# Kernel tuning notes

Hardware: AMD Instinct MI355X
Metric: run time of the kernel (lower is better)

The kernel has to match this reference:

```python
import jax, jax.numpy as jnp
import numpy as np
import math

B, C, HW = 4, 256, 32          # batch, seq_len (=channels), spatial side
D_MODEL = HW * HW              # 1024
OUT_C = 32 * 32                # 1024
D_STATE = 16
EXPAND = 2
D_INNER = EXPAND * D_MODEL     # 2048
DT_RANK = math.ceil(D_MODEL / 16)  # 64
D_CONV = 4


def setup_inputs() -> dict:
    key = jax.random.key(0)
    ks = jax.random.split(key, 12)
    s = 0.02
    x1 = jax.random.normal(ks[0], (B, C, HW, HW), dtype=jnp.float32)
    in_proj_w = jax.random.normal(ks[1], (2 * D_INNER, D_MODEL), dtype=jnp.float32) * s
    conv_w = jax.random.normal(ks[2], (D_INNER, 1, D_CONV), dtype=jnp.float32) * s
    conv_b = jnp.zeros((D_INNER,), dtype=jnp.float32)
    x_proj_w = jax.random.normal(ks[3], (DT_RANK + 2 * D_STATE, D_INNER), dtype=jnp.float32) * s
    dt_proj_w = jax.random.normal(ks[4], (D_INNER, DT_RANK), dtype=jnp.float32) * s
    dt_proj_b = jnp.zeros((D_INNER,), dtype=jnp.float32)
    A_log = jnp.log(jnp.broadcast_to(jnp.arange(1, D_STATE + 1, dtype=jnp.float32), (D_INNER, D_STATE)))
    D = jnp.ones((D_INNER,), dtype=jnp.float32)
    out_proj_w = jax.random.normal(ks[5], (OUT_C, D_INNER), dtype=jnp.float32) * s
    ln_w = jnp.ones((OUT_C,), dtype=jnp.float32)
    ln_b = jnp.zeros((OUT_C,), dtype=jnp.float32)
    return {"x1": x1, "in_proj_w": in_proj_w, "conv_w": conv_w, "conv_b": conv_b,
            "x_proj_w": x_proj_w, "dt_proj_w": dt_proj_w, "dt_proj_b": dt_proj_b,
            "A_log": A_log, "D": D, "out_proj_w": out_proj_w, "ln_w": ln_w, "ln_b": ln_b}


def _mamba_forward(x, in_proj_w, conv_w, conv_b, x_proj_w, dt_proj_w, dt_proj_b, A_log, D, out_proj_w):
    # x: (B, L, d_model)
    xz = jnp.einsum('bld,ed->ble', x, in_proj_w)            # (B,L,2*d_inner)
    xs, res = jnp.split(xz, 2, axis=-1)                     # each (B,L,d_inner)
    # depthwise causal conv1d, padding=d_conv-1 then truncate to L (== left pad)
    xs_c = jnp.transpose(xs, (0, 2, 1))                     # (B,d_inner,L)
    xs_c = jax.lax.conv_general_dilated(
        xs_c, conv_w, window_strides=(1,), padding=[(D_CONV - 1, 0)],
        dimension_numbers=('NCH', 'OIH', 'NCH'), feature_group_count=D_INNER)
    xs_c = xs_c + conv_b[None, :, None]
    xs = jax.nn.silu(jnp.transpose(xs_c, (0, 2, 1)))        # (B,L,d_inner)
    # input-dependent SSM parameters
    x_dbl = jnp.einsum('bld,ed->ble', xs, x_proj_w)         # (B,L,dt_rank+2N)
    dt, Bm, Cm = jnp.split(x_dbl, [DT_RANK, DT_RANK + D_STATE], axis=-1)
    delta = jax.nn.softplus(jnp.einsum('blr,dr->bld', dt, dt_proj_w) + dt_proj_b)  # (B,L,d_inner)
    A = -jnp.exp(A_log)                                     # (d_inner, N)
    deltaA = jnp.exp(delta[..., None] * A)                  # (B,L,d_inner,N)
    deltaB_u = delta[..., None] * Bm[:, :, None, :] * xs[..., None]  # (B,L,d_inner,N)

    def step(h, inp):
        dA, dBu, Ct = inp                                   # (B,d,N),(B,d,N),(B,N)
        h = dA * h + dBu
        y = jnp.einsum('bdn,bn->bd', h, Ct)
        return h, y

    h0 = jnp.zeros((deltaA.shape[0], D_INNER, D_STATE), dtype=deltaA.dtype)
    _, ys = jax.lax.scan(step, h0, (jnp.transpose(deltaA, (1, 0, 2, 3)),
                                    jnp.transpose(deltaB_u, (1, 0, 2, 3)),
                                    jnp.transpose(Cm, (1, 0, 2))))
    y = jnp.transpose(ys, (1, 0, 2))                        # (B,L,d_inner)
    y = y + D * xs
    y = y * jax.nn.silu(res)
    return jnp.einsum('bld,od->blo', y, out_proj_w)         # (B,L,out_c)


def reference(x1, in_proj_w, conv_w, conv_b, x_proj_w, dt_proj_w, dt_proj_b,
              A_log, D, out_proj_w, ln_w, ln_b):
    b, c, h, w = x1.shape
    x = x1.reshape(b, c, h * w)                             # (B, L=c, d_model)
    y = _mamba_forward(x, in_proj_w, conv_w, conv_b, x_proj_w, dt_proj_w,
                       dt_proj_b, A_log, D, out_proj_w)
    mu = jnp.mean(y, axis=-1, keepdims=True)
    var = jnp.var(y, axis=-1, keepdims=True)
    y = (y - mu) * jax.lax.rsqrt(var + 1e-5) * ln_w + ln_b
    return y.reshape(b, c, 32, 32)
```

## Files before the change

### kernel.cpp

```cpp
#include <hip/hip_runtime.h>
#include <hip/hip_bf16.h>
#include <math.h>

#define BATCH 4
#define SEQL 256
#define DMODEL 1024
#define DINNER 2048
#define DSTATE 16
#define OUTC 1024
#define NROWS (BATCH * SEQL)
#define NCHUNK 4
#define CH 64
#define XPZ 16

typedef __attribute__((ext_vector_type(8))) short bf16x8;
typedef __attribute__((ext_vector_type(4))) float f32x4;

__global__ __launch_bounds__(256) void gemm_mfma(const __hip_bfloat16* __restrict__ A,
                                                 const __hip_bfloat16* __restrict__ B,
                                                 float* __restrict__ C,
                                                 int M, int N, int K,
                                                 int lda, int ldb) {
    __shared__ __hip_bfloat16 As[4][128 * 32];
    __shared__ __hip_bfloat16 Bs[4][128 * 32];
    const int t  = threadIdx.x;
    const int w  = t >> 6;
    const int ln = t & 63;
    const int wm = w >> 1, wn = w & 1;
    const int q  = ln >> 4, lr = ln & 15;
    const int m0 = blockIdx.y * 128;
    const int n0 = blockIdx.x * 128;
    const int Kpart = K / gridDim.z;
    const int kbase = blockIdx.z * Kpart;

    f32x4 acc[4][4] = {};

    const __hip_bfloat16* Ag = A + (size_t)m0 * lda + kbase;
    const __hip_bfloat16* Bg = B + (size_t)n0 * ldb + kbase;

    auto stage = [&](int k0, int buf) {
        #pragma unroll
        for (int i = 0; i < 2; ++i) {
            const int c = (i * 4 + w) * 64 + ln;
            const int r = c >> 2, col = (c & 3) * 8;
            __builtin_amdgcn_global_load_lds(
                (const __attribute__((address_space(1))) void*)(Ag + (size_t)r * lda + k0 + col),
                (__attribute__((address_space(3))) void*)(As[buf] + (i * 4 + w) * 64 * 8),
                16, 0, 0);
            __builtin_amdgcn_global_load_lds(
                (const __attribute__((address_space(1))) void*)(Bg + (size_t)r * ldb + k0 + col),
                (__attribute__((address_space(3))) void*)(Bs[buf] + (i * 4 + w) * 64 * 8),
                16, 0, 0);
        }
    };

    const int nk = Kpart / 32;
    for (int s = 0; s < 3 && s < nk; ++s) stage(s * 32, s);

    for (int kk = 0; kk < nk; ++kk) {
        const int last = (kk + 2 < nk - 1) ? (kk + 2) : (nk - 1);
        const int nf = last - kk;
        if (nf >= 2)      asm volatile("s_waitcnt vmcnt(8)" ::: "memory");
        else if (nf == 1) asm volatile("s_waitcnt vmcnt(4)" ::: "memory");
        else              asm volatile("s_waitcnt vmcnt(0)" ::: "memory");
        __builtin_amdgcn_s_barrier();
        if (kk + 3 < nk) stage((kk + 3) * 32, (kk + 3) & 3);

        const int buf = kk & 3;
        bf16x8 af[4], bfr[4];
        #pragma unroll
        for (int i = 0; i < 4; ++i)
            af[i] = *(const bf16x8*)(As[buf] + (wm * 64 + i * 16 + lr) * 32 + q * 8);
        #pragma unroll
        for (int j = 0; j < 4; ++j)
            bfr[j] = *(const bf16x8*)(Bs[buf] + (wn * 64 + j * 16 + lr) * 32 + q * 8);
        #pragma unroll
        for (int i = 0; i < 4; ++i)
            #pragma unroll
            for (int j = 0; j < 4; ++j)
                acc[i][j] = __builtin_amdgcn_mfma_f32_16x16x32_bf16(af[i], bfr[j], acc[i][j], 0, 0, 0);
    }
    float* Cz = C + (size_t)blockIdx.z * M * N;
    #pragma unroll
    for (int i = 0; i < 4; ++i) {
        const int mrow = m0 + wm * 64 + i * 16 + q * 4;
        #pragma unroll
        for (int j = 0; j < 4; ++j) {
            const int ncol = n0 + wn * 64 + j * 16 + lr;
            #pragma unroll
            for (int r = 0; r < 4; ++r)
                Cz[(size_t)(mrow + r) * N + ncol] = acc[i][j][r];
        }
    }
}

__global__ __launch_bounds__(256) void xproj_conv(const float* __restrict__ xz,
                                                  const float* __restrict__ conv_w,
                                                  const float* __restrict__ conv_b,
                                                  const __hip_bfloat16* __restrict__ Wp,
                                                  float* __restrict__ xpart) {
    __shared__ __hip_bfloat16 As[4 * 4096];
    __shared__ __hip_bfloat16 Bs[4 * 4096];
    const int t  = threadIdx.x;
    const int w  = t >> 6;
    const int ln = t & 63;
    const int wm = w >> 1, wn = w & 1;
    const int q  = ln >> 4, lr = ln & 15;
    const int z  = blockIdx.x;
    const int m0 = blockIdx.y * 128;
    const int kbase = z * 128;

    const __hip_bfloat16* Bg = Wp + kbase;
    #pragma unroll
    for (int stg = 0; stg < 4; ++stg) {
        #pragma unroll
        for (int i = 0; i < 2; ++i) {
            const int c = (i * 4 + w) * 64 + ln;
            const int r = c >> 2, col = (c & 3) * 8;
            __builtin_amdgcn_global_load_lds(
                (const __attribute__((address_space(1))) void*)(Bg + (size_t)r * 2048 + stg * 32 + col),
                (__attribute__((address_space(3))) void*)(Bs + stg * 4096 + (i * 4 + w) * 512),
                16, 0, 0);
        }
    }

    {
        const int r  = t >> 1;
        const int dh = (t & 1) * 16;
        const int gr = m0 + r;
        const int bb = gr >> 8, l = gr & 255;
        const float* xrow = xz + (size_t)bb * 256 * 4096;
        #pragma unroll
        for (int stg = 0; stg < 4; ++stg) {
            const int d0 = kbase + stg * 32 + dh;
            #pragma unroll
            for (int j = 0; j < 4; ++j) {
                const int d = d0 + j * 4;
                float4 t0 = {}, t1 = {}, t2 = {}, t3;
                if (l >= 3) t0 = *(const float4*)(xrow + (size_t)(l - 3) * 4096 + d);
                if (l >= 2) t1 = *(const float4*)(xrow + (size_t)(l - 2) * 4096 + d);
                if (l >= 1) t2 = *(const float4*)(xrow + (size_t)(l - 1) * 4096 + d);
                t3 = *(const float4*)(xrow + (size_t)l * 4096 + d);
                const float* p0 = (const float*)&t0;
                const float* p1 = (const float*)&t1;
                const float* p2 = (const float*)&t2;
                const float* p3 = (const float*)&t3;
                #pragma unroll
                for (int u = 0; u < 4; ++u) {
                    const int du = d + u;
                    const float4 wv = *(const float4*)(conv_w + (size_t)du * 4);
                    float acc = conv_b[du];
                    if (l >= 3) acc += wv.x * p0[u];
                    if (l >= 2) acc += wv.y * p1[u];
                    if (l >= 1) acc += wv.z * p2[u];
                    acc += wv.w * p3[u];
                    const float v = acc / (1.f + __expf(-acc));
                    As[stg * 4096 + r * 32 + dh + j * 4 + u] = __float2bfloat16(v);
                }
            }
        }
    }
    __syncthreads();

    f32x4 acc[4][4] = {};
    #pragma unroll
    for (int kk = 0; kk < 4; ++kk) {
        const __hip_bfloat16* Ab = As + kk * 4096;
        const __hip_bfloat16* Bb = Bs + kk * 4096;
        bf16x8 af[4], bfr[4];
        #pragma unroll
        for (int i = 0; i < 4; ++i)
            af[i] = *(const bf16x8*)(Ab + (wm * 64 + i * 16 + lr) * 32 + q * 8);
        #pragma unroll
        for (int j = 0; j < 4; ++j)
            bfr[j] = *(const bf16x8*)(Bb + (wn * 64 + j * 16 + lr) * 32 + q * 8);
        #pragma unroll
        for (int i = 0; i < 4; ++i)
            #pragma unroll
            for (int j = 0; j < 4; ++j)
                acc[i][j] = __builtin_amdgcn_mfma_f32_16x16x32_bf16(af[i], bfr[j], acc[i][j], 0, 0, 0);
    }
    float* Cz = xpart + (size_t)z * (1024 * 128);
    #pragma unroll
    for (int i = 0; i < 4; ++i) {
        const int mrow = m0 + wm * 64 + i * 16 + q * 4;
        #pragma unroll
        for (int j = 0; j < 4; ++j) {
            const int ncol = wn * 64 + j * 16 + lr;
            #pragma unroll
            for (int r = 0; r < 4; ++r)
                Cz[(size_t)(mrow + r) * 128 + ncol] = acc[i][j][r];
        }
    }
}

__global__ __launch_bounds__(256) void gemm_dtsp(const __hip_bfloat16* __restrict__ A,
                                                 const __hip_bfloat16* __restrict__ B,
                                                 const float* __restrict__ bd,
                                                 float* __restrict__ delta) {
    __shared__ __hip_bfloat16 As[2][128 * 32];
    __shared__ __hip_bfloat16 Bs[2][128 * 32];
    const int t  = threadIdx.x;
    const int w  = t >> 6;
    const int ln = t & 63;
    const int wm = w >> 1, wn = w & 1;
    const int q  = ln >> 4, lr = ln & 15;
    const int m0 = blockIdx.y * 128;
    const int n0 = blockIdx.x * 128;
    const int lda = 128, ldb = 64, N = 2048;

    f32x4 acc[4][4] = {};
    const __hip_bfloat16* Ag = A + (size_t)m0 * lda;
    const __hip_bfloat16* Bg = B + (size_t)n0 * ldb;

    auto stage = [&](int k0, int buf) {
        #pragma unroll
        for (int i = 0; i < 2; ++i) {
            const int c = (i * 4 + w) * 64 + ln;
            const int r = c >> 2, col = (c & 3) * 8;
            __builtin_amdgcn_global_load_lds(
                (const __attribute__((address_space(1))) void*)(Ag + (size_t)r * lda + k0 + col),
                (__attribute__((address_space(3))) void*)(As[buf] + (i * 4 + w) * 64 * 8),
                16, 0, 0);
            __builtin_amdgcn_global_load_lds(
                (const __attribute__((address_space(1))) void*)(Bg + (size_t)r * ldb + k0 + col),
                (__attribute__((address_space(3))) void*)(Bs[buf] + (i * 4 + w) * 64 * 8),
                16, 0, 0);
        }
    };

    stage(0, 0);
    stage(32, 1);
    #pragma unroll
    for (int kk = 0; kk < 2; ++kk) {
        if (kk == 0) asm volatile("s_waitcnt vmcnt(4)" ::: "memory");
        else         asm volatile("s_waitcnt vmcnt(0)" ::: "memory");
        __builtin_amdgcn_s_barrier();
        bf16x8 af[4], bfr[4];
        #pragma unroll
        for (int i = 0; i < 4; ++i)
            af[i] = *(const bf16x8*)(As[kk] + (wm * 64 + i * 16 + lr) * 32 + q * 8);
        #pragma unroll
        for (int j = 0; j < 4; ++j)
            bfr[j] = *(const bf16x8*)(Bs[kk] + (wn * 64 + j * 16 + lr) * 32 + q * 8);
        #pragma unroll
        for (int i = 0; i < 4; ++i)
            #pragma unroll
            for (int j = 0; j < 4; ++j)
                acc[i][j] = __builtin_amdgcn_mfma_f32_16x16x32_bf16(af[i], bfr[j], acc[i][j], 0, 0, 0);
    }
    #pragma unroll
    for (int i = 0; i < 4; ++i) {
        const int mrow = m0 + wm * 64 + i * 16 + q * 4;
        #pragma unroll
        for (int j = 0; j < 4; ++j) {
            const int ncol = n0 + wn * 64 + j * 16 + lr;
            const float bias = bd[ncol];
            #pragma unroll
            for (int r = 0; r < 4; ++r) {
                float v = acc[i][j][r] + bias;
                float sp = (v > 20.f) ? v : log1pf(__expf(v));
                delta[(size_t)(mrow + r) * N + ncol] = sp;
            }
        }
    }
}

__global__ void xdbl_reduce_kernel(const float* __restrict__ part,
                                   float* __restrict__ xdbl,
                                   __hip_bfloat16* __restrict__ xdblb) {
    const int i = blockIdx.x * 256 + threadIdx.x;
    float s = 0.f;
    #pragma unroll
    for (int z = 0; z < XPZ; ++z) s += part[(size_t)z * (1024 * 128) + i];
    xdbl[i] = s;
    xdblb[i] = __float2bfloat16(s);
}

#define R0 (1024 * 1024)
#define R1 (R0 + 4096 * 1024)
#define R2 (R1 + 2048 * 1024)
#define R3 (R2 + 128 * 2048)
#define R4 (R3 + 2048 * 64)
__global__ void cast_all_kernel(const float* __restrict__ x1,
                                const float* __restrict__ w_in,
                                const float* __restrict__ w_out,
                                const float* __restrict__ w_xp,
                                const float* __restrict__ w_dt,
                                __hip_bfloat16* __restrict__ xa,
                                __hip_bfloat16* __restrict__ wb1,
                                __hip_bfloat16* __restrict__ wob,
                                __hip_bfloat16* __restrict__ wpb,
                                __hip_bfloat16* __restrict__ wdb) {
    int i = blockIdx.x * 256 + threadIdx.x;
    if (i < R0) {
        xa[i] = __float2bfloat16(x1[i]);
    } else if (i < R1) {
        int j = i - R0; wb1[j] = __float2bfloat16(w_in[j]);
    } else if (i < R2) {
        int j = i - R1; wob[j] = __float2bfloat16(w_out[j]);
    } else if (i < R3) {
        int j = i - R2; int e = j >> 11;
        wpb[j] = __float2bfloat16(e < 96 ? w_xp[j] : 0.f);
    } else if (i < R4) {
        int j = i - R3; wdb[j] = __float2bfloat16(w_dt[j]);
    }
}

__device__ __forceinline__ float row_reduce16(float x) {
    x += __int_as_float(__builtin_amdgcn_update_dpp(0, __float_as_int(x), 0x128, 0xF, 0xF, true));
    x += __int_as_float(__builtin_amdgcn_update_dpp(0, __float_as_int(x), 0x124, 0xF, 0xF, true));
    x += __int_as_float(__builtin_amdgcn_update_dpp(0, __float_as_int(x), 0x122, 0xF, 0xF, true));
    x += __int_as_float(__builtin_amdgcn_update_dpp(0, __float_as_int(x), 0x121, 0xF, 0xF, true));
    return x;
}

__global__ __launch_bounds__(256) void scan_fused(const float* __restrict__ delta,
                                                  const float* __restrict__ xz,
                                                  const float* __restrict__ conv_w,
                                                  const float* __restrict__ conv_b,
                                                  const float* __restrict__ xdbl,
                                                  const float* __restrict__ A_log,
                                                  const float* __restrict__ Dp,
                                                  __hip_bfloat16* __restrict__ ybb) {
    __shared__ float sDU[CH][16][2];
    __shared__ float sBC[CH][16][2];
    __shared__ float sGW[CH][16][2];
    const int b = blockIdx.y, dg = blockIdx.x;
    const int t = threadIdx.x;
    const int dl = t >> 4, n = t & 15;
    const int d = dg * 16 + dl;
    const float a = -__expf(A_log[d * DSTATE + n]);
    const int srow = t >> 4, scol = t & 15;
    const int sd = dg * 16 + scol;
    const float Dstage = Dp[sd];
    const float cb = conv_b[sd];
    const float w0 = conv_w[sd * 4 + 0];
    const float w1 = conv_w[sd * 4 + 1];
    const float w2 = conv_w[sd * 4 + 2];
    const float w3 = conv_w[sd * 4 + 3];
    const float* xbase = xz + (size_t)(b * SEQL) * 4096 + sd;

    float h = 0.f;
    for (int c = 0; c < NCHUNK; ++c) {
        const int rowbase = b * SEQL + c * CH;
        __syncthreads();
        #pragma unroll
        for (int i = 0; i < 4; ++i) {
            const int row = rowbase + i * 16 + srow;
            const int l = row & (SEQL - 1);
            const float dv = delta[(size_t)row * DINNER + sd];
            float acc = cb;
            if (l >= 3) acc += w0 * xbase[(size_t)(l - 3) * 4096];
            if (l >= 2) acc += w1 * xbase[(size_t)(l - 2) * 4096];
            if (l >= 1) acc += w2 * xbase[(size_t)(l - 1) * 4096];
            acc += w3 * xbase[(size_t)l * 4096];
            const float xv = acc / (1.f + __expf(-acc));
            const float r  = xz[(size_t)row * 4096 + DINNER + sd];
            const float g = r / (1.f + __expf(-r));
            const int lr_ = i * 16 + srow;
            sDU[lr_][scol][0] = dv;
            sDU[lr_][scol][1] = dv * xv;
            sGW[lr_][scol][0] = g;
            sGW[lr_][scol][1] = Dstage * xv * g;
            sBC[lr_][scol][0] = xdbl[row * 128 + 64 + scol];
            sBC[lr_][scol][1] = xdbl[row * 128 + 80 + scol];
        }
        __syncthreads();
        #pragma unroll 16
        for (int l = 0; l < CH; ++l) {
            const float e = __expf(sDU[l][dl][0] * a);
            h = e * h + sDU[l][dl][1] * sBC[l][n][0];
            float pr = row_reduce16(h * sBC[l][n][1]);
            if (n == 0) {
                const float y = pr * sGW[l][dl][0] + sGW[l][dl][1];
                ybb[(size_t)(rowbase + l) * DINNER + d] = __float2bfloat16(y);
            }
        }
    }
}

__global__ __launch_bounds__(256) void ln_kernel(const float* __restrict__ opart,
                                                 const float* __restrict__ lw,
                                                 const float* __restrict__ lb,
                                                 float* __restrict__ out) {
    __shared__ float red[8];
    const int row = blockIdx.x;
    const int t = threadIdx.x;
    float v[4];
    float s = 0.f, s2 = 0.f;
    #pragma unroll
    for (int i = 0; i < 4; ++i) {
        const int c = t + 256 * i;
        float acc = 0.f;
        #pragma unroll
        for (int z = 0; z < 4; ++z)
            acc += opart[(size_t)z * (1024 * 1024) + (size_t)row * OUTC + c];
        v[i] = acc;
        s += acc;
        s2 += acc * acc;
    }
    #pragma unroll
    for (int o = 32; o; o >>= 1) {
        s += __shfl_down(s, o);
        s2 += __shfl_down(s2, o);
    }
    const int wid = t >> 6;
    if ((t & 63) == 0) { red[wid] = s; red[4 + wid] = s2; }
    __syncthreads();
    if (t == 0) {
        float ts = red[0] + red[1] + red[2] + red[3];
        float ts2 = red[4] + red[5] + red[6] + red[7];
        float mu = ts * (1.f / OUTC);
        float var = ts2 * (1.f / OUTC) - mu * mu;
        red[0] = mu;
        red[1] = rsqrtf(var + 1e-5f);
    }
    __syncthreads();
    const float mu = red[0], rs = red[1];
    #pragma unroll
    for (int i = 0; i < 4; ++i) {
        const int c = t + 256 * i;
        out[(size_t)row * OUTC + c] = (v[i] - mu) * rs * lw[c] + lb[c];
    }
}

extern "C" void kernel_launch(void* const* d_in, const int* in_sizes, int n_in,
                              void* d_out, int out_size, void* d_ws, size_t ws_size,
                              hipStream_t stream) {
    const float* x1        = (const float*)d_in[0];
    const float* in_proj_w = (const float*)d_in[1];
    const float* conv_w    = (const float*)d_in[2];
    const float* conv_b    = (const float*)d_in[3];
    const float* x_proj_w  = (const float*)d_in[4];
    const float* dt_proj_w = (const float*)d_in[5];
    const float* dt_proj_b = (const float*)d_in[6];
    const float* A_log     = (const float*)d_in[7];
    const float* Dp        = (const float*)d_in[8];
    const float* out_proj_w= (const float*)d_in[9];
    const float* ln_w      = (const float*)d_in[10];
    const float* ln_b      = (const float*)d_in[11];
    float* out = (float*)d_out;

    char* p = (char*)d_ws;
    __hip_bfloat16* xa    = (__hip_bfloat16*)p; p += (size_t)1024 * 1024 * 2;
    __hip_bfloat16* wb1   = (__hip_bfloat16*)p; p += (size_t)4096 * 1024 * 2;
    __hip_bfloat16* wpb   = (__hip_bfloat16*)p; p += (size_t)128 * 2048 * 2;
    __hip_bfloat16* wob   = (__hip_bfloat16*)p; p += (size_t)1024 * 2048 * 2;
    __hip_bfloat16* wdb   = (__hip_bfloat16*)p; p += (size_t)2048 * 64 * 2;
    __hip_bfloat16* ybb   = (__hip_bfloat16*)p; p += (size_t)1024 * 2048 * 2;
    __hip_bfloat16* xdblb = (__hip_bfloat16*)p; p += (size_t)1024 * 128 * 2;
    float* xz    = (float*)p; p += (size_t)1024 * 4096 * 4;
    float* xdbl  = (float*)p; p += (size_t)1024 * 128 * 4;
    float* xpart = (float*)p; p += (size_t)XPZ * 1024 * 128 * 4;
    float* delta = (float*)p; p += (size_t)1024 * 2048 * 4;
    float* opart = xz;

    cast_all_kernel<<<(R4 + 255) / 256, 256, 0, stream>>>(x1, in_proj_w, out_proj_w,
                                                          x_proj_w, dt_proj_w,
                                                          xa, wb1, wob, wpb, wdb);
    gemm_mfma<<<dim3(32, 8, 1), 256, 0, stream>>>(xa, wb1, xz,
                                                  NROWS, 2 * DINNER, DMODEL, DMODEL, DMODEL);
    xproj_conv<<<dim3(XPZ, 8), 256, 0, stream>>>(xz, conv_w, conv_b, wpb, xpart);
    xdbl_reduce_kernel<<<(1024 * 128) / 256, 256, 0, stream>>>(xpart, xdbl, xdblb);
    gemm_dtsp<<<dim3(16, 8), 256, 0, stream>>>(xdblb, wdb, dt_proj_b, delta);
    scan_fused<<<dim3(DINNER / 16, BATCH), 256, 0, stream>>>(
        delta, xz, conv_w, conv_b, xdbl, A_log, Dp, ybb);
    gemm_mfma<<<dim3(8, 8, 4), 256, 0, stream>>>(ybb, wob, opart,
                                                 NROWS, OUTC, DINNER, DINNER, DINNER);
    ln_kernel<<<NROWS, 256, 0, stream>>>(opart, ln_w, ln_b, out);
}
```

Baseline: 237.3 us.

## Parallelize selective scan across chunks, vectorize casts, swizzle GEMM block order

The sequential per-block chunk loop of the scan is split into two kernels. The first computes each chunk's local end state and decay product in parallel. The second combines the preceding chunk carries and rescans its own chunk, which gives four times more blocks at the cost of recomputing the conv, silu and exp work. The cast kernel now converts four floats per thread with vector loads and stores. GEMM workgroup ids are remapped with an XCD-style swizzle to improve cache locality.

```diff
diff --git a/kernel.cpp b/kernel.cpp
--- a/kernel.cpp
+++ b/kernel.cpp
@@ -28,8 +28,11 @@
     const int ln = t & 63;
     const int wm = w >> 1, wn = w & 1;
     const int q  = ln >> 4, lr = ln & 15;
-    const int m0 = blockIdx.y * 128;
-    const int n0 = blockIdx.x * 128;
+    const int id  = blockIdx.y * gridDim.x + blockIdx.x;
+    const int nwg = gridDim.x * gridDim.y;
+    const int sid = (id & 7) * (nwg >> 3) + (id >> 3);
+    const int m0 = (sid / gridDim.x) * 128;
+    const int n0 = (sid % gridDim.x) * 128;
     const int Kpart = K / gridDim.z;
     const int kbase = blockIdx.z * Kpart;
 
@@ -282,6 +285,20 @@
 #define R2 (R1 + 2048 * 1024)
 #define R3 (R2 + 128 * 2048)
 #define R4 (R3 + 2048 * 64)
+
+__device__ __forceinline__ ushort4 cvt4(float4 v) {
+    __hip_bfloat16 h0 = __float2bfloat16(v.x);
+    __hip_bfloat16 h1 = __float2bfloat16(v.y);
+    __hip_bfloat16 h2 = __float2bfloat16(v.z);
+    __hip_bfloat16 h3 = __float2bfloat16(v.w);
+    ushort4 o;
+    o.x = *reinterpret_cast<unsigned short*>(&h0);
+    o.y = *reinterpret_cast<unsigned short*>(&h1);
+    o.z = *reinterpret_cast<unsigned short*>(&h2);
+    o.w = *reinterpret_cast<unsigned short*>(&h3);
+    return o;
+}
+
 __global__ void cast_all_kernel(const float* __restrict__ x1,
                                 const float* __restrict__ w_in,
                                 const float* __restrict__ w_out,
@@ -292,18 +309,23 @@
                                 __hip_bfloat16* __restrict__ wob,
                                 __hip_bfloat16* __restrict__ wpb,
                                 __hip_bfloat16* __restrict__ wdb) {
-    int i = blockIdx.x * 256 + threadIdx.x;
+    const int i = (blockIdx.x * 256 + threadIdx.x) * 4;
+    if (i >= R4) return;
     if (i < R0) {
-        xa[i] = __float2bfloat16(x1[i]);
+        *reinterpret_cast<ushort4*>(xa + i) = cvt4(*(const float4*)(x1 + i));
     } else if (i < R1) {
-        int j = i - R0; wb1[j] = __float2bfloat16(w_in[j]);
+        int j = i - R0;
+        *reinterpret_cast<ushort4*>(wb1 + j) = cvt4(*(const float4*)(w_in + j));
     } else if (i < R2) {
-        int j = i - R1; wob[j] = __float2bfloat16(w_out[j]);
+        int j = i - R1;
+        *reinterpret_cast<ushort4*>(wob + j) = cvt4(*(const float4*)(w_out + j));
     } else if (i < R3) {
         int j = i - R2; int e = j >> 11;
-        wpb[j] = __float2bfloat16(e < 96 ? w_xp[j] : 0.f);
-    } else if (i < R4) {
-        int j = i - R3; wdb[j] = __float2bfloat16(w_dt[j]);
+        float4 v = (e < 96) ? *(const float4*)(w_xp + j) : float4{0.f, 0.f, 0.f, 0.f};
+        *reinterpret_cast<ushort4*>(wpb + j) = cvt4(v);
+    } else {
+        int j = i - R3;
+        *reinterpret_cast<ushort4*>(wdb + j) = cvt4(*(const float4*)(w_dt + j));
     }
 }
 
@@ -315,18 +337,72 @@
     return x;
 }
 
-__global__ __launch_bounds__(256) void scan_fused(const float* __restrict__ delta,
-                                                  const float* __restrict__ xz,
-                                                  const float* __restrict__ conv_w,
-                                                  const float* __restrict__ conv_b,
-                                                  const float* __restrict__ xdbl,
-                                                  const float* __restrict__ A_log,
-                                                  const float* __restrict__ Dp,
-                                                  __hip_bfloat16* __restrict__ ybb) {
+__global__ __launch_bounds__(256) void scan_carry_kernel(const float* __restrict__ delta,
+                                                         const float* __restrict__ xz,
+                                                         const float* __restrict__ conv_w,
+                                                         const float* __restrict__ conv_b,
+                                                         const float* __restrict__ xdbl,
+                                                         const float* __restrict__ A_log,
+                                                         float* __restrict__ carryL,
+                                                         float* __restrict__ carryP) {
+    __shared__ float sDU[CH][16][2];
+    __shared__ float sB[CH][16];
+    const int b = blockIdx.y, c = blockIdx.z, dg = blockIdx.x;
+    const int t = threadIdx.x;
+    const int dl = t >> 4, n = t & 15;
+    const int d = dg * 16 + dl;
+    const float a = -__expf(A_log[d * DSTATE + n]);
+    const int srow = t >> 4, scol = t & 15;
+    const int sd = dg * 16 + scol;
+    const float cb = conv_b[sd];
+    const float w0 = conv_w[sd * 4 + 0];
+    const float w1 = conv_w[sd * 4 + 1];
+    const float w2 = conv_w[sd * 4 + 2];
+    const float w3 = conv_w[sd * 4 + 3];
+    const float* xbase = xz + (size_t)(b * SEQL) * 4096 + sd;
+    const int rowbase = b * SEQL + c * CH;
+    #pragma unroll
+    for (int i = 0; i < 4; ++i) {
+        const int row = rowbase + i * 16 + srow;
+        const int l = row & (SEQL - 1);
+        const float dv = delta[(size_t)row * DINNER + sd];
+        float acc = cb;
+        if (l >= 3) acc += w0 * xbase[(size_t)(l - 3) * 4096];
+        if (l >= 2) acc += w1 * xbase[(size_t)(l - 2) * 4096];
+        if (l >= 1) acc += w2 * xbase[(size_t)(l - 1) * 4096];
+        acc += w3 * xbase[(size_t)l * 4096];
+        const float xv = acc / (1.f + __expf(-acc));
+        sDU[i * 16 + srow][scol][0] = dv;
+        sDU[i * 16 + srow][scol][1] = dv * xv;
+        sB[i * 16 + srow][scol] = xdbl[row * 128 + 64 + scol];
+    }
+    __syncthreads();
+    float h = 0.f, P = 1.f;
+    #pragma unroll 16
+    for (int l = 0; l < CH; ++l) {
+        const float e = __expf(sDU[l][dl][0] * a);
+        h = e * h + sDU[l][dl][1] * sB[l][n];
+        P *= e;
+    }
+    const size_t ci = (((size_t)(b * NCHUNK + c)) * DINNER + d) * DSTATE + n;
+    carryL[ci] = h;
+    carryP[ci] = P;
+}
+
+__global__ __launch_bounds__(256) void scan_apply_kernel(const float* __restrict__ delta,
+                                                         const float* __restrict__ xz,
+                                                         const float* __restrict__ conv_w,
+                                                         const float* __restrict__ conv_b,
+                                                         const float* __restrict__ xdbl,
+                                                         const float* __restrict__ A_log,
+                                                         const float* __restrict__ Dp,
+                                                         const float* __restrict__ carryL,
+                                                         const float* __restrict__ carryP,
+                                                         __hip_bfloat16* __restrict__ ybb) {
     __shared__ float sDU[CH][16][2];
     __shared__ float sBC[CH][16][2];
     __shared__ float sGW[CH][16][2];
-    const int b = blockIdx.y, dg = blockIdx.x;
+    const int b = blockIdx.y, c = blockIdx.z, dg = blockIdx.x;
     const int t = threadIdx.x;
     const int dl = t >> 4, n = t & 15;
     const int d = dg * 16 + dl;
@@ -340,42 +416,42 @@
     const float w2 = conv_w[sd * 4 + 2];
     const float w3 = conv_w[sd * 4 + 3];
     const float* xbase = xz + (size_t)(b * SEQL) * 4096 + sd;
-
+    const int rowbase = b * SEQL + c * CH;
+    #pragma unroll
+    for (int i = 0; i < 4; ++i) {
+        const int row = rowbase + i * 16 + srow;
+        const int l = row & (SEQL - 1);
+        const float dv = delta[(size_t)row * DINNER + sd];
+        float acc = cb;
+        if (l >= 3) acc += w0 * xbase[(size_t)(l - 3) * 4096];
+        if (l >= 2) acc += w1 * xbase[(size_t)(l - 2) * 4096];
+        if (l >= 1) acc += w2 * xbase[(size_t)(l - 1) * 4096];
+        acc += w3 * xbase[(size_t)l * 4096];
+        const float xv = acc / (1.f + __expf(-acc));
+        const float r  = xz[(size_t)row * 4096 + DINNER + sd];
+        const float g = r / (1.f + __expf(-r));
+        const int lr_ = i * 16 + srow;
+        sDU[lr_][scol][0] = dv;
+        sDU[lr_][scol][1] = dv * xv;
+        sGW[lr_][scol][0] = g;
+        sGW[lr_][scol][1] = Dstage * xv * g;
+        sBC[lr_][scol][0] = xdbl[row * 128 + 64 + scol];
+        sBC[lr_][scol][1] = xdbl[row * 128 + 80 + scol];
+    }
+    __syncthreads();
     float h = 0.f;
-    for (int c = 0; c < NCHUNK; ++c) {
-        const int rowbase = b * SEQL + c * CH;
-        __syncthreads();
-        #pragma unroll
-        for (int i = 0; i < 4; ++i) {
-            const int row = rowbase + i * 16 + srow;
-            const int l = row & (SEQL - 1);
-            const float dv = delta[(size_t)row * DINNER + sd];
-            float acc = cb;
-            if (l >= 3) acc += w0 * xbase[(size_t)(l - 3) * 4096];
-            if (l >= 2) acc += w1 * xbase[(size_t)(l - 2) * 4096];
-            if (l >= 1) acc += w2 * xbase[(size_t)(l - 1) * 4096];
-            acc += w3 * xbase[(size_t)l * 4096];
-            const float xv = acc / (1.f + __expf(-acc));
-            const float r  = xz[(size_t)row * 4096 + DINNER + sd];
-            const float g = r / (1.f + __expf(-r));
-            const int lr_ = i * 16 + srow;
-            sDU[lr_][scol][0] = dv;
-            sDU[lr_][scol][1] = dv * xv;
-            sGW[lr_][scol][0] = g;
-            sGW[lr_][scol][1] = Dstage * xv * g;
-            sBC[lr_][scol][0] = xdbl[row * 128 + 64 + scol];
-            sBC[lr_][scol][1] = xdbl[row * 128 + 80 + scol];
-        }
-        __syncthreads();
-        #pragma unroll 16
-        for (int l = 0; l < CH; ++l) {
-            const float e = __expf(sDU[l][dl][0] * a);
-            h = e * h + sDU[l][dl][1] * sBC[l][n][0];
-            float pr = row_reduce16(h * sBC[l][n][1]);
-            if (n == 0) {
-                const float y = pr * sGW[l][dl][0] + sGW[l][dl][1];
-                ybb[(size_t)(rowbase + l) * DINNER + d] = __float2bfloat16(y);
-            }
+    for (int j = 0; j < c; ++j) {
+        const size_t ci = (((size_t)(b * NCHUNK + j)) * DINNER + d) * DSTATE + n;
+        h = carryP[ci] * h + carryL[ci];
+    }
+    #pragma unroll 16
+    for (int l = 0; l < CH; ++l) {
+        const float e = __expf(sDU[l][dl][0] * a);
+        h = e * h + sDU[l][dl][1] * sBC[l][n][0];
+        float pr = row_reduce16(h * sBC[l][n][1]);
+        if (n == 0) {
+            const float y = pr * sGW[l][dl][0] + sGW[l][dl][1];
+            ybb[(size_t)(rowbase + l) * DINNER + d] = __float2bfloat16(y);
         }
     }
 }
@@ -454,18 +530,22 @@
     float* xdbl  = (float*)p; p += (size_t)1024 * 128 * 4;
     float* xpart = (float*)p; p += (size_t)XPZ * 1024 * 128 * 4;
     float* delta = (float*)p; p += (size_t)1024 * 2048 * 4;
+    float* carryL = (float*)p; p += (size_t)BATCH * NCHUNK * DINNER * DSTATE * 4;
+    float* carryP = (float*)p; p += (size_t)BATCH * NCHUNK * DINNER * DSTATE * 4;
     float* opart = xz;
 
-    cast_all_kernel<<<(R4 + 255) / 256, 256, 0, stream>>>(x1, in_proj_w, out_proj_w,
-                                                          x_proj_w, dt_proj_w,
-                                                          xa, wb1, wob, wpb, wdb);
+    cast_all_kernel<<<(R4 / 4 + 255) / 256, 256, 0, stream>>>(x1, in_proj_w, out_proj_w,
+                                                              x_proj_w, dt_proj_w,
+                                                              xa, wb1, wob, wpb, wdb);
     gemm_mfma<<<dim3(32, 8, 1), 256, 0, stream>>>(xa, wb1, xz,
                                                   NROWS, 2 * DINNER, DMODEL, DMODEL, DMODEL);
     xproj_conv<<<dim3(XPZ, 8), 256, 0, stream>>>(xz, conv_w, conv_b, wpb, xpart);
     xdbl_reduce_kernel<<<(1024 * 128) / 256, 256, 0, stream>>>(xpart, xdbl, xdblb);
     gemm_dtsp<<<dim3(16, 8), 256, 0, stream>>>(xdblb, wdb, dt_proj_b, delta);
-    scan_fused<<<dim3(DINNER / 16, BATCH), 256, 0, stream>>>(
-        delta, xz, conv_w, conv_b, xdbl, A_log, Dp, ybb);
+    scan_carry_kernel<<<dim3(DINNER / 16, BATCH, NCHUNK - 1), 256, 0, stream>>>(
+        delta, xz, conv_w, conv_b, xdbl, A_log, carryL, carryP);
+    scan_apply_kernel<<<dim3(DINNER / 16, BATCH, NCHUNK), 256, 0, stream>>>(
+        delta, xz, conv_w, conv_b, xdbl, A_log, Dp, carryL, carryP, ybb);
     gemm_mfma<<<dim3(8, 8, 4), 256, 0, stream>>>(ybb, wob, opart,
                                                  NROWS, OUTC, DINNER, DINNER, DINNER);
     ln_kernel<<<NROWS, 256, 0, stream>>>(opart, ln_w, ln_b, out);
```

Result: faster. 227.6 us (-4.1%).
